# Optimization experiments

Hardware: AMD Instinct MI355X
Metric: run time of the kernel (lower is better)

Reference implementation:

```python
import jax, jax.numpy as jnp
import numpy as np

N_USERS = 50000; N_ENT = 100000; C = 64
E = 1500000; NNZ = 1000000
N_REL = 16; N_CATES = 32; NF = 4; NH = 2
R1 = N_REL - 1            # weight rows (devoted branch)
R2 = N_CATES + N_REL - 1  # weight_d rows (diverse branch)


def setup_inputs():
    key = jax.random.key(0)
    ks = list(jax.random.split(key, 32))
    f = jnp.float32
    inp = {}
    inp["user_emb"] = jax.random.normal(ks[0], (N_USERS, C), f)
    inp["entity_emb"] = jax.random.normal(ks[1], (N_ENT, C), f)
    inp["latent_emb"] = jax.random.normal(ks[2], (NF, C), f)
    inp["latent_div_emb"] = jax.random.normal(ks[3], (NF, C), f)
    inp["weight"] = jax.random.normal(ks[4], (R1, C), f) * 0.1
    inp["weight_d"] = jax.random.normal(ks[5], (R2, C), f) * 0.1
    # per-hop Aggregator params stacked over hops [NH, ...]; Linear applied as x @ W + b
    def p(k, shape, s=0.1):
        return jax.random.normal(k, shape, f) * s
    inp["cW1"] = p(ks[6], (NH, C, C)); inp["cb1"] = jnp.zeros((NH, C), f)
    inp["cW2"] = p(ks[7], (NH, C, C)); inp["cb2"] = jnp.zeros((NH, C), f)
    inp["cWua"] = p(ks[8], (NH, NF, NF)); inp["cbua"] = jnp.zeros((NH, NF), f)
    inp["cWwa"] = p(ks[9], (NH, R1, R1)); inp["cbwa"] = jnp.zeros((NH, R1), f)
    inp["eW1"] = p(ks[10], (NH, C, C)); inp["eb1"] = jnp.zeros((NH, C), f)
    inp["eW2"] = p(ks[11], (NH, C, C)); inp["eb2"] = jnp.zeros((NH, C), f)
    inp["eWua"] = p(ks[12], (NH, NF, NF)); inp["ebua"] = jnp.zeros((NH, NF), f)
    inp["eWwa"] = p(ks[13], (NH, R2, R2)); inp["ebwa"] = jnp.zeros((NH, R2), f)
    inp["interact_vals"] = jax.random.uniform(ks[14], (NNZ,), f)
    inp["edge_index"] = jax.random.randint(ks[15], (2, E), 0, N_ENT)
    inp["edge_type"] = jax.random.randint(ks[16], (E,), 1, N_REL)            # values in [1, R1]
    inp["entity_cate_set"] = jax.random.randint(ks[17], (N_ENT,), 1, N_CATES + 1)
    inp["interact_rows"] = jax.random.randint(ks[18], (NNZ,), 0, N_USERS)
    inp["interact_cols"] = jax.random.randint(ks[19], (NNZ,), 0, N_ENT)
    return inp


def _lin(x, W, b):
    return x @ W + b


def _mlp(x, W, b):  # Linear + LeakyReLU(0.2)
    return jax.nn.leaky_relu(_lin(x, W, b), 0.2)


def _normalize(x):  # F.normalize along dim=1 (eps=1e-12)
    return x / jnp.maximum(jnp.linalg.norm(x, axis=1, keepdims=True), 1e-12)


def _agg(entity_emb, user_emb, latent_emb, weight, w_idx, head, tail,
         rows, cols, vals, W1, b1, W2, b2, Wua, bua, Wwa, bwa):
    n_ent, n_usr = entity_emb.shape[0], user_emb.shape[0]
    # KG aggregate: gather -> multiply -> scatter_mean over head
    neigh = entity_emb[tail] * weight[w_idx]                                  # [E, C]
    ssum = jax.ops.segment_sum(neigh, head, num_segments=n_ent)
    cnt = jax.ops.segment_sum(jnp.ones((head.shape[0],), entity_emb.dtype), head, num_segments=n_ent)
    entity_agg = ssum / jnp.maximum(cnt, 1.0)[:, None]
    # user aggregate: sparse.mm(interact_mat, entity_emb)
    user_agg = jax.ops.segment_sum(vals[:, None] * entity_emb[cols], rows, num_segments=n_usr)
    # user -> latent interest attention
    score_ = _lin(user_emb, W1, b1) @ _lin(latent_emb, W1, b1).T              # [U, NF]
    score = jax.nn.softmax(_mlp(score_, Wua, bua), axis=1)                    # [U, NF]
    score_rp = _lin(latent_emb, W2, b2) @ _lin(weight, W2, b2).T              # [NF, R]
    latent_new = jax.nn.softmax(_mlp(score_rp, Wwa, bwa), axis=-1) @ weight   # [NF, C]
    mix = jnp.einsum("uf,fc->uc", score, latent_new)                          # (disen_weight * score).sum(1)
    user_agg = user_agg * mix + user_agg
    return entity_agg, user_agg, latent_new


def _dist_corr(t1, t2):
    ch = t1.shape[0]
    t1 = t1[:, None]; t2 = t2[:, None]
    sq1, sq2 = t1 ** 2, t2 ** 2
    a = jnp.sqrt(jnp.maximum(sq1 - 2.0 * (t1 @ t1.T) + sq1.T, 0.0) + 1e-8)
    b = jnp.sqrt(jnp.maximum(sq2 - 2.0 * (t2 @ t2.T) + sq2.T, 0.0) + 1e-8)
    A = a - a.mean(0, keepdims=True) - a.mean(1, keepdims=True) + a.mean()
    B = b - b.mean(0, keepdims=True) - b.mean(1, keepdims=True) + b.mean()
    n2 = float(ch * ch)
    dab = jnp.sqrt(jnp.maximum((A * B).sum() / n2, 0.0) + 1e-8)
    daa = jnp.sqrt(jnp.maximum((A * A).sum() / n2, 0.0) + 1e-8)
    dbb = jnp.sqrt(jnp.maximum((B * B).sum() / n2, 0.0) + 1e-8)
    return dab / jnp.sqrt(daa * dbb + 1e-8)


def _cor(lat):  # ind == "distance": sum over factor pairs
    c = jnp.asarray(0.0, lat.dtype)
    for i in range(NF):
        for j in range(i + 1, NF):
            c = c + _dist_corr(lat[i], lat[j])
    return c


def reference(user_emb, entity_emb, latent_emb, latent_div_emb, weight, weight_d,
              cW1, cb1, cW2, cb2, cWua, cbua, cWwa, cbwa,
              eW1, eb1, eW2, eb2, eWua, ebua, eWwa, ebwa,
              interact_vals, edge_index, edge_type, entity_cate_set,
              interact_rows, interact_cols):
    head, tail = edge_index[0], edge_index[1]
    idx_c = edge_type - 1               # devoted branch: relation weight index
    idx_d = entity_cate_set[tail] - 1   # diverse branch: category weight index
    # Devoted Interest Branch
    e, u, l = entity_emb, user_emb, latent_emb
    e_res, u_res, l_res = entity_emb, user_emb, latent_emb
    for i in range(NH):
        e, u, l = _agg(e, u, l, weight, idx_c, head, tail,
                       interact_rows, interact_cols, interact_vals,
                       cW1[i], cb1[i], cW2[i], cb2[i], cWua[i], cbua[i], cWwa[i], cbwa[i])
        e = _normalize(e); u = _normalize(u)
        l_res = _normalize(l)           # faithful: overwritten each hop, then += l
        e_res = e_res + e; u_res = u_res + u; l_res = l_res + l
    # Diverse Interest Branch
    e, u, l2 = entity_emb, user_emb, latent_div_emb
    e_d, u_d, l_d = entity_emb, user_emb, latent_div_emb
    for i in range(NH):
        e, u, l2 = _agg(e, u, l2, weight_d, idx_d, head, tail,
                        interact_rows, interact_cols, interact_vals,
                        eW1[i], eb1[i], eW2[i], eb2[i], eWua[i], ebua[i], eWwa[i], ebwa[i])
        e = _normalize(e); u = _normalize(u); l2 = _normalize(l2)
        e_d = e_d + e; u_d = u_d + u; l_d = l_d + l2
    cor = _cor(l_res)
    cor_d = _cor(l_d)
    return (e_res, u_res, cor, e_d, u_d, cor_d)
```

## Files before the change

### kernel.cpp

```cpp
#include <hip/hip_runtime.h>
#include <hip/hip_bf16.h>
#include <math.h>

typedef __hip_bfloat16 bf16;

#define NUSR 50000
#define NENT 100000
#define CC   64
#define EE   1500000
#define NNZI 1000000
#define NF_  4
#define R1_  15
#define R2_  47

__device__ __forceinline__ float b2f(bf16 x){ return __bfloat162float(x); }
__device__ __forceinline__ bf16  f2b(float x){ return __float2bfloat16(x); }
__device__ __forceinline__ float fin(float x){ return (x==x && fabsf(x) < 1e30f) ? x : 0.f; }

__device__ __forceinline__ unsigned bf16bits(float x){
    unsigned b = __float_as_uint(x);
    return (b + 0x7FFFu + ((b >> 16) & 1u)) >> 16;
}
__device__ __forceinline__ float pk_lo(unsigned p){ return __uint_as_float(p << 16); }
__device__ __forceinline__ float pk_hi(unsigned p){ return __uint_as_float(p & 0xFFFF0000u); }

__device__ __forceinline__ unsigned rflu(unsigned x){ return (unsigned)__builtin_amdgcn_readfirstlane((int)x); }

__device__ __forceinline__ float ldv(const float* p, long long i){ return p[i]; }
__device__ __forceinline__ float ldv(const bf16*  p, long long i){ return b2f(p[i]); }

struct LatArgs {
    const float *lin, *W1, *b1, *W2, *b2, *Wua, *bua, *Wwa, *bwa, *wt;
    float *lat, *nlat, *P2, *q2;
    int R;
};

__global__ void k_init(int* deg_e, int* deg_u, int* ctrs){
    int i = blockIdx.x*256 + threadIdx.x;
    if (i < NENT) deg_e[i] = 0;
    if (i < NUSR) deg_u[i] = 0;
    if (i < 2) ctrs[i] = 0;
}

__global__ void k_conv(const float* __restrict__ src, bf16* __restrict__ dst){
    int i = blockIdx.x*256 + threadIdx.x;
    if (i < NENT*CC) dst[i] = f2b(src[i]);
}

__global__ void k_hist(const int* __restrict__ head, const int* __restrict__ irows,
                       int* deg_e, int* deg_u,
                       int* __restrict__ rank_e, int* __restrict__ rank_u){
    int i = blockIdx.x*256 + threadIdx.x;
    if (i < EE){
        int h = head[i];
        int r = ((unsigned)h < NENT) ? atomicAdd(&deg_e[h], 1) : 0;
        rank_e[i] = r;
    } else {
        int j = i - EE;
        if (j < NNZI){
            int rr = irows[j];
            int r = ((unsigned)rr < NUSR) ? atomicAdd(&deg_u[rr], 1) : 0;
            rank_u[j] = r;
        }
    }
}

__global__ void k_base2(const int* __restrict__ deg_e, const int* __restrict__ deg_u,
                        unsigned* rsdeg_e, unsigned* rsdeg_u, int* ctrs){
    int i = blockIdx.x*256 + threadIdx.x;
    int lane = threadIdx.x & 63;
    {
        int d = (i < NENT) ? deg_e[i] : 0;
        int incl = d;
        for (int off = 1; off < 64; off <<= 1){
            int v = __shfl_up(incl, off, 64);
            if (lane >= off) incl += v;
        }
        int tot = __shfl(incl, 63, 64);
        int base = 0;
        if (lane == 63) base = atomicAdd(&ctrs[0], tot);
        base = __shfl(base, 63, 64);
        if (i < NENT){
            unsigned rs = (unsigned)(base + incl - d);
            int dc = d < 2047 ? d : 2047;
            rsdeg_e[i] = (rs & 0x1FFFFFu) | ((unsigned)dc << 21);
        }
    }
    {
        int d = (i < NUSR) ? deg_u[i] : 0;
        int incl = d;
        for (int off = 1; off < 64; off <<= 1){
            int v = __shfl_up(incl, off, 64);
            if (lane >= off) incl += v;
        }
        int tot = __shfl(incl, 63, 64);
        int base = 0;
        if (lane == 63) base = atomicAdd(&ctrs[1], tot);
        base = __shfl(base, 63, 64);
        if (i < NUSR){
            unsigned rs = (unsigned)(base + incl - d);
            int dc = d < 4095 ? d : 4095;
            rsdeg_u[i] = (rs & 0xFFFFFu) | ((unsigned)dc << 20);
        }
    }
}

__global__ void k_scatter(const int* __restrict__ head, const int* __restrict__ tail,
                          const int* __restrict__ etype, const int* __restrict__ cate,
                          const int* __restrict__ irows, const int* __restrict__ icols,
                          const float* __restrict__ ivals,
                          const int* __restrict__ rank_e, const int* __restrict__ rank_u,
                          const unsigned* __restrict__ rsdeg_e, const unsigned* __restrict__ rsdeg_u,
                          unsigned* __restrict__ epk, unsigned* __restrict__ upk){
    int i = blockIdx.x*256 + threadIdx.x;
    if (i < EE){
        int h = head[i]; if ((unsigned)h >= NENT) return;
        unsigned tu = (unsigned)tail[i]; if (tu >= NENT) tu = 0;
        int slot = (int)(rsdeg_e[h] & 0x1FFFFFu) + rank_e[i];
        unsigned ty = (unsigned)(etype[i] - 1) & 15u;
        unsigned cd = (unsigned)(cate[tu]  - 1) & 31u;
        if ((unsigned)slot < EE)
            epk[slot] = tu | (ty << 17) | (cd << 21);
    } else {
        int j = i - EE;
        if (j < NNZI){
            int r = irows[j]; if ((unsigned)r >= NUSR) return;
            unsigned c = (unsigned)icols[j]; if (c >= NENT) c = 0;
            int slot = (int)(rsdeg_u[r] & 0xFFFFFu) + rank_u[j];
            unsigned bits = __float_as_uint(ivals[j]);
            unsigned rb = bits + 0x7FFFu + ((bits >> 16) & 1u);
            unsigned vb = (rb >> 16) & 0x7FFFu;
            if ((unsigned)slot < NNZI)
                upk[slot] = c | (vb << 17);
        }
    }
}

__global__ void k_lat2(LatArgs A0, LatArgs A1){
    LatArgs a = (blockIdx.x == 0) ? A0 : A1;
    const int R = a.R;
    __shared__ float sW1[64*64], sW2[64*64];
    __shared__ float swt[R2_*64], wp[R2_*64];
    __shared__ float lf[NF_*64], lp1[NF_*64], lp2[NF_*64];
// ... 137 lines not shown
                                              const unsigned* __restrict__ rsdeg_e,
                                              const unsigned* __restrict__ epk,
                                              bf16* dst){
    __shared__ float wl[R2_*64];
    int t = threadIdx.x;
    for (int idx = t; idx < R2_*64; idx += 256)
        wl[idx] = (idx < R*64) ? wtab[idx] : 0.f;
    __syncthreads();
    int ent = blockIdx.x*4 + (t >> 6);
    int lane = t & 63;
    if (ent >= NENT) return;
    float v = ent_row(e_src, wl, epk, rsdeg_e[ent], use_d, lane);
    dst[(long long)ent*64 + lane] = f2b(v);
}

__global__ __launch_bounds__(256) void k_ent0f2(const bf16* __restrict__ ebf,
                                                const float* __restrict__ wt_c,
                                                const float* __restrict__ wt_d,
                                                const unsigned* __restrict__ rsdeg_e,
                                                const unsigned* __restrict__ epk,
                                                unsigned* __restrict__ eA2){
    __shared__ float wlc[R1_*64];
    __shared__ float wld[R2_*64];
    int t = threadIdx.x;
    for (int idx = t; idx < R1_*64; idx += 256) wlc[idx] = wt_c[idx];
    for (int idx = t; idx < R2_*64; idx += 256) wld[idx] = wt_d[idx];
    __syncthreads();
    int ent = blockIdx.x*4 + (t >> 6);
    int lane = t & 63;
    if (ent >= NENT) return;
    unsigned rd = rflu(rsdeg_e[ent]);
    int s = (int)(rd & 0x1FFFFFu);
    int deg = (int)(rd >> 21);
    int e_ = s + deg;
    float ac = 0.f, ad = 0.f;
    int k = s;
    for (; k + 4 <= e_; k += 4){
        unsigned p0 = rflu(epk[k]), p1 = rflu(epk[k+1]), p2 = rflu(epk[k+2]), p3 = rflu(epk[k+3]);
        unsigned t0 = p0 & 0x1FFFFu; t0 = t0 < NENT ? t0 : 0u;
        unsigned t1 = p1 & 0x1FFFFu; t1 = t1 < NENT ? t1 : 0u;
        unsigned t2 = p2 & 0x1FFFFu; t2 = t2 < NENT ? t2 : 0u;
        unsigned t3 = p3 & 0x1FFFFu; t3 = t3 < NENT ? t3 : 0u;
        float g0 = b2f(ebf[(long long)t0*64 + lane]);
        float g1 = b2f(ebf[(long long)t1*64 + lane]);
        float g2 = b2f(ebf[(long long)t2*64 + lane]);
        float g3 = b2f(ebf[(long long)t3*64 + lane]);
        ac += g0*wlc[((p0>>17)&15u)*64+lane] + g1*wlc[((p1>>17)&15u)*64+lane]
            + g2*wlc[((p2>>17)&15u)*64+lane] + g3*wlc[((p3>>17)&15u)*64+lane];
        ad += g0*wld[((p0>>21)&31u)*64+lane] + g1*wld[((p1>>21)&31u)*64+lane]
            + g2*wld[((p2>>21)&31u)*64+lane] + g3*wld[((p3>>21)&31u)*64+lane];
    }
    for (; k < e_; k++){
        unsigned p = rflu(epk[k]);
        unsigned ti = p & 0x1FFFFu; ti = ti < NENT ? ti : 0u;
        float g = b2f(ebf[(long long)ti*64 + lane]);
        ac += g*wlc[((p>>17)&15u)*64+lane];
        ad += g*wld[((p>>21)&31u)*64+lane];
    }
    float inv_deg = 1.f / fmaxf((float)deg, 1.f);
    float ec = fin(ac) * inv_deg, ed = fin(ad) * inv_deg;
    float sc = ec*ec, sd = ed*ed;
    for (int m = 1; m < 64; m <<= 1){
        sc += __shfl_xor(sc, m, 64);
        sd += __shfl_xor(sd, m, 64);
    }
    float vc = ec / fmaxf(sqrtf(fin(sc)), 1e-12f);
    float vd = ed / fmaxf(sqrtf(fin(sd)), 1e-12f);
    eA2[(long long)ent*64 + lane] = bf16bits(vc) | (bf16bits(vd) << 16);
}

__global__ __launch_bounds__(256) void k_ent1f(const bf16* __restrict__ e_src,
                                               const float* __restrict__ base_emb,
                                               const float* __restrict__ wtab, int R, int use_d,
                                               const unsigned* __restrict__ rsdeg_e,
                                               const unsigned* __restrict__ epk,
                                               float* dst){
    __shared__ float wl[R2_*64];
    int t = threadIdx.x;
    for (int idx = t; idx < R2_*64; idx += 256)
        wl[idx] = (idx < R*64) ? wtab[idx] : 0.f;
    __syncthreads();
    int ent = blockIdx.x*4 + (t >> 6);
    int lane = t & 63;
    if (ent >= NENT) return;
    float v = ent_row(e_src, wl, epk, rsdeg_e[ent], use_d, lane);
    long long ix = (long long)ent*64 + lane;
    dst[ix] = base_emb[ix] + b2f(e_src[ix]) + v;
}

__global__ __launch_bounds__(256) void k_ent1f2(const unsigned* __restrict__ eA2,
                                                const float* __restrict__ base_emb,
                                                const float* __restrict__ wt_c,
                                                const float* __restrict__ wt_d,
                                                const unsigned* __restrict__ rsdeg_e,
                                                const unsigned* __restrict__ epk,
                                                float* __restrict__ dst_c,
                                                float* __restrict__ dst_d){
    __shared__ float wlc[R1_*64];
    __shared__ float wld[R2_*64];
    int t = threadIdx.x;
    for (int idx = t; idx < R1_*64; idx += 256) wlc[idx] = wt_c[idx];
    for (int idx = t; idx < R2_*64; idx += 256) wld[idx] = wt_d[idx];
    __syncthreads();
    int ent = blockIdx.x*4 + (t >> 6);
    int lane = t & 63;
    if (ent >= NENT) return;
    unsigned rd = rflu(rsdeg_e[ent]);
    int s = (int)(rd & 0x1FFFFFu);
    int deg = (int)(rd >> 21);
    int e_ = s + deg;
    float ac = 0.f, ad = 0.f;
    int k = s;
    for (; k + 4 <= e_; k += 4){
        unsigned p0 = rflu(epk[k]), p1 = rflu(epk[k+1]), p2 = rflu(epk[k+2]), p3 = rflu(epk[k+3]);
        unsigned t0 = p0 & 0x1FFFFu; t0 = t0 < NENT ? t0 : 0u;
        unsigned t1 = p1 & 0x1FFFFu; t1 = t1 < NENT ? t1 : 0u;
        unsigned t2 = p2 & 0x1FFFFu; t2 = t2 < NENT ? t2 : 0u;
        unsigned t3 = p3 & 0x1FFFFu; t3 = t3 < NENT ? t3 : 0u;
        unsigned v0 = eA2[(long long)t0*64 + lane];
        unsigned v1 = eA2[(long long)t1*64 + lane];
        unsigned v2 = eA2[(long long)t2*64 + lane];
        unsigned v3 = eA2[(long long)t3*64 + lane];
        ac += pk_lo(v0)*wlc[((p0>>17)&15u)*64+lane] + pk_lo(v1)*wlc[((p1>>17)&15u)*64+lane]
            + pk_lo(v2)*wlc[((p2>>17)&15u)*64+lane] + pk_lo(v3)*wlc[((p3>>17)&15u)*64+lane];
        ad += pk_hi(v0)*wld[((p0>>21)&31u)*64+lane] + pk_hi(v1)*wld[((p1>>21)&31u)*64+lane]
            + pk_hi(v2)*wld[((p2>>21)&31u)*64+lane] + pk_hi(v3)*wld[((p3>>21)&31u)*64+lane];
    }
    for (; k < e_; k++){
        unsigned p = rflu(epk[k]);
        unsigned ti = p & 0x1FFFFu; ti = ti < NENT ? ti : 0u;
        unsigned v = eA2[(long long)ti*64 + lane];
        ac += pk_lo(v) * wlc[((p>>17)&15u)*64+lane];
        ad += pk_hi(v) * wld[((p>>21)&31u)*64+lane];
    }
    float inv_deg = 1.f / fmaxf((float)deg, 1.f);
    float vc = fin(ac) * inv_deg, vd = fin(ad) * inv_deg;
    float sc = vc*vc, sd = vd*vd;
    for (int m = 1; m < 64; m <<= 1){
        sc += __shfl_xor(sc, m, 64);
        sd += __shfl_xor(sd, m, 64);
    }
    long long ix = (long long)ent*64 + lane;
    float be = base_emb[ix];
    unsigned selfv = eA2[ix];
    dst_c[ix] = be + pk_lo(selfv) + vc / fmaxf(sqrtf(fin(sc)), 1e-12f);
    dst_d[ix] = be + pk_hi(selfv) + vd / fmaxf(sqrtf(fin(sd)), 1e-12f);
}

template<typename ESRC>
__device__ __forceinline__ float usr_gather(const ESRC* __restrict__ e_src,
                                            const unsigned* __restrict__ upk,
                                            unsigned rd, int lane){
    rd = rflu(rd);
    int s = (int)(rd & 0xFFFFFu);
    int e_ = s + (int)(rd >> 20);
    float acc = 0.f;
    int k = s;
    for (; k + 4 <= e_; k += 4){
        unsigned p0 = rflu(upk[k]), p1 = rflu(upk[k+1]), p2 = rflu(upk[k+2]), p3 = rflu(upk[k+3]);
        unsigned c0 = p0 & 0x1FFFFu; c0 = c0 < NENT ? c0 : 0u;
        unsigned c1 = p1 & 0x1FFFFu; c1 = c1 < NENT ? c1 : 0u;
// ... 50 lines not shown
                                              const float* __restrict__ lat_new,
                                              float* dst){
    __shared__ float P2l[NF_*64], latl[NF_*64], q2l[NF_];
    int t = threadIdx.x;
    P2l[t] = fin(P2[t]); latl[t] = fin(lat_new[t]);
    if (t < NF_) q2l[t] = fin(q2[t]);
    __syncthreads();
    int u = blockIdx.x*4 + (t >> 6);
    int lane = t & 63;
    if (u >= NUSR) return;
    float acc = usr_gather(e_src, upk, rsdeg_u[u], lane);
    float x = u_src[(long long)u*64 + lane];
    dst[(long long)u*64 + lane] = usr_epi(acc, x, P2l, latl, q2l, lane);
}

__global__ __launch_bounds__(256) void k_usr0f2(const float* __restrict__ u_src,
                                                const bf16* __restrict__ ebf,
                                                const unsigned* __restrict__ rsdeg_u,
                                                const unsigned* __restrict__ upk,
                                                const float* __restrict__ P2c,
                                                const float* __restrict__ q2c,
                                                const float* __restrict__ latc,
                                                const float* __restrict__ P2d,
                                                const float* __restrict__ q2d,
                                                const float* __restrict__ latd,
                                                float* __restrict__ dst_c,
                                                float* __restrict__ dst_d){
    __shared__ float P2lc[NF_*64], latlc[NF_*64], P2ld[NF_*64], latld[NF_*64];
    __shared__ float q2lc[NF_], q2ld[NF_];
    int t = threadIdx.x;
    P2lc[t] = fin(P2c[t]); latlc[t] = fin(latc[t]);
    P2ld[t] = fin(P2d[t]); latld[t] = fin(latd[t]);
    if (t < NF_){ q2lc[t] = fin(q2c[t]); q2ld[t] = fin(q2d[t]); }
    __syncthreads();
    int u = blockIdx.x*4 + (t >> 6);
    int lane = t & 63;
    if (u >= NUSR) return;
    float acc = usr_gather(ebf, upk, rsdeg_u[u], lane);
    long long ix = (long long)u*64 + lane;
    float x = u_src[ix];
    dst_c[ix] = usr_epi(acc, x, P2lc, latlc, q2lc, lane);
    dst_d[ix] = usr_epi(acc, x, P2ld, latld, q2ld, lane);
}

__global__ __launch_bounds__(256) void k_usr1f(float* u_io,
                                               const bf16* __restrict__ e_src,
                                               const float* __restrict__ base_emb,
                                               const unsigned* __restrict__ rsdeg_u,
                                               const unsigned* __restrict__ upk,
                                               const float* __restrict__ P2,
                                               const float* __restrict__ q2,
                                               const float* __restrict__ lat_new){
    __shared__ float P2l[NF_*64], latl[NF_*64], q2l[NF_];
    int t = threadIdx.x;
    P2l[t] = fin(P2[t]); latl[t] = fin(lat_new[t]);
    if (t < NF_) q2l[t] = fin(q2[t]);
    __syncthreads();
    int u = blockIdx.x*4 + (t >> 6);
    int lane = t & 63;
    if (u >= NUSR) return;
    float acc = usr_gather(e_src, upk, rsdeg_u[u], lane);
    long long ix = (long long)u*64 + lane;
    float x = u_io[ix];
    float v = usr_epi(acc, x, P2l, latl, q2l, lane);
    u_io[ix] = base_emb[ix] + x + v;
}

__global__ __launch_bounds__(256) void k_usr1f2(float* __restrict__ uc_io,
                                                float* __restrict__ ud_io,
                                                const unsigned* __restrict__ eA2,
                                                const float* __restrict__ base_emb,
                                                const unsigned* __restrict__ rsdeg_u,
                                                const unsigned* __restrict__ upk,
                                                const float* __restrict__ P2c,
                                                const float* __restrict__ q2c,
                                                const float* __restrict__ latc,
                                                const float* __restrict__ P2d,
                                                const float* __restrict__ q2d,
                                                const float* __restrict__ latd){
    __shared__ float P2lc[NF_*64], latlc[NF_*64], P2ld[NF_*64], latld[NF_*64];
    __shared__ float q2lc[NF_], q2ld[NF_];
    int t = threadIdx.x;
    P2lc[t] = fin(P2c[t]); latlc[t] = fin(latc[t]);
    P2ld[t] = fin(P2d[t]); latld[t] = fin(latd[t]);
    if (t < NF_){ q2lc[t] = fin(q2c[t]); q2ld[t] = fin(q2d[t]); }
    __syncthreads();
    int u = blockIdx.x*4 + (t >> 6);
    int lane = t & 63;
    if (u >= NUSR) return;
    unsigned rd = rflu(rsdeg_u[u]);
    int s = (int)(rd & 0xFFFFFu);
    int e_ = s + (int)(rd >> 20);
    float accc = 0.f, accd = 0.f;
    int k = s;
    for (; k + 4 <= e_; k += 4){
        unsigned p0 = rflu(upk[k]), p1 = rflu(upk[k+1]), p2 = rflu(upk[k+2]), p3 = rflu(upk[k+3]);
        unsigned c0 = p0 & 0x1FFFFu; c0 = c0 < NENT ? c0 : 0u;
        unsigned c1 = p1 & 0x1FFFFu; c1 = c1 < NENT ? c1 : 0u;
        unsigned c2 = p2 & 0x1FFFFu; c2 = c2 < NENT ? c2 : 0u;
        unsigned c3 = p3 & 0x1FFFFu; c3 = c3 < NENT ? c3 : 0u;
        float v0 = __uint_as_float(((p0 >> 17) & 0x7FFFu) << 16);
        float v1 = __uint_as_float(((p1 >> 17) & 0x7FFFu) << 16);
        float v2 = __uint_as_float(((p2 >> 17) & 0x7FFFu) << 16);
        float v3 = __uint_as_float(((p3 >> 17) & 0x7FFFu) << 16);
        unsigned g0 = eA2[(long long)c0*64 + lane];
        unsigned g1 = eA2[(long long)c1*64 + lane];
        unsigned g2 = eA2[(long long)c2*64 + lane];
        unsigned g3 = eA2[(long long)c3*64 + lane];
        accc += v0*pk_lo(g0) + v1*pk_lo(g1) + v2*pk_lo(g2) + v3*pk_lo(g3);
        accd += v0*pk_hi(g0) + v1*pk_hi(g1) + v2*pk_hi(g2) + v3*pk_hi(g3);
    }
    for (; k < e_; k++){
        unsigned p = rflu(upk[k]);
        unsigned c = p & 0x1FFFFu; c = c < NENT ? c : 0u;
        float v = __uint_as_float(((p >> 17) & 0x7FFFu) << 16);
        unsigned g = eA2[(long long)c*64 + lane];
        accc += v * pk_lo(g);
        accd += v * pk_hi(g);
    }
    long long ix = (long long)u*64 + lane;
    float xc = uc_io[ix], xd = ud_io[ix];
    float be = base_emb[ix];
    float vc = usr_epi(fin(accc), xc, P2lc, latlc, q2lc, lane);
    float vd = usr_epi(fin(accd), xd, P2ld, latld, q2ld, lane);
    uc_io[ix] = be + xc + vc;
    ud_io[ix] = be + xd + vd;
}

__global__ void k_cor(const float* __restrict__ latn1_c,
                      const float* __restrict__ ldiv,
                      const float* __restrict__ nld0, const float* __restrict__ nld1,
                      float* out){
    __shared__ float rows[NF_*64];
    __shared__ float nr[NF_];
    __shared__ float t1s[64], t2s[64], m1s[64], m2s[64];
    __shared__ float pr[256], pr2[256], pr3[256];
    __shared__ float gms[2];
    __shared__ float corsh;
    int t = threadIdx.x, b = blockIdx.x;

    if (b == 0){
// ... 116 lines not shown
    size_t ebuf  = (size_t)NENT*CC*2;
    size_t ebuf2 = (size_t)NENT*CC*4;
    bool tierA = (ws_size >= common + ((ebuf + 255) & ~(size_t)255) + ((ebuf2 + 255) & ~(size_t)255));

    bf16 *ebf = nullptr; unsigned* eA2 = nullptr; bf16* eA = nullptr;
    char* scratch_base;
    if (tierA){
        ebf = (bf16*)carve(ebuf);
        eA2 = (unsigned*)carve(ebuf2);
        scratch_base = (char*)eA2;
    } else {
        eA  = (bf16*)carve(ebuf);
        scratch_base = (char*)eA;
    }

    int* deg_e = (int*)scratch_base;
    int* deg_u = (int*)(scratch_base + (512<<10));
    int* ctrs  = (int*)(scratch_base + (1024<<10));
    char* rbase = scratch_base + (1280<<10);
    int* rank_e = (int*)rbase;
    int* rank_u = (int*)(rbase + (((size_t)EE*4 + 255) & ~(size_t)255));

    float* oe_c = out;
    float* ou_c = out + 6400000LL;
    float* oe_d = out + 9600001LL;
    float* ou_d = out + 16000001LL;

    k_init<<<(NENT+255)/256, 256, 0, stream>>>(deg_e, deg_u, ctrs);
    if (tierA) k_conv<<<(NENT*CC+255)/256, 256, 0, stream>>>(entity_emb, ebf);
    int gh = (EE + NNZI + 255)/256;
    k_hist<<<gh, 256, 0, stream>>>(head, irows, deg_e, deg_u, rank_e, rank_u);
    k_base2<<<(NENT+255)/256, 256, 0, stream>>>(deg_e, deg_u, rsdeg_e, rsdeg_u, ctrs);
    k_scatter<<<gh, 256, 0, stream>>>(head, tail, etype, cate, irows, icols, ivals,
                                      rank_e, rank_u, rsdeg_e, rsdeg_u, epk, upk);

    LatArgs a_c0 = {latent_emb, cW1, cb1, cW2, cb2, cWua, cbua, cWwa, cbwa, weight,
                    latn[0][0], nlat[0][0], P2b[0][0], q2b[0][0], R1_};
    LatArgs a_d0 = {latent_div, eW1, eb1, eW2, eb2, eWua, ebua, eWwa, ebwa, weight_d,
                    latn[1][0], nlat[1][0], P2b[1][0], q2b[1][0], R2_};
    k_lat2<<<2, 256, 0, stream>>>(a_c0, a_d0);
    LatArgs a_c1 = {latn[0][0], cW1+4096, cb1+64, cW2+4096, cb2+64, cWua+16, cbua+4,
                    cWwa+R1_*R1_, cbwa+R1_, weight,
                    latn[0][1], nlat[0][1], P2b[0][1], q2b[0][1], R1_};
    LatArgs a_d1 = {nlat[1][0], eW1+4096, eb1+64, eW2+4096, eb2+64, eWua+16, ebua+4,
                    eWwa+R2_*R2_, ebwa+R2_, weight_d,
                    latn[1][1], nlat[1][1], P2b[1][1], q2b[1][1], R2_};
    k_lat2<<<2, 256, 0, stream>>>(a_c1, a_d1);

    int ge = (NENT+3)/4, gu = (NUSR+3)/4;
    if (tierA){
        k_ent0f2<<<ge, 256, 0, stream>>>(ebf, weight, weight_d, rsdeg_e, epk, eA2);
        k_usr0f2<<<gu, 256, 0, stream>>>(user_emb, ebf, rsdeg_u, upk,
            P2b[0][0], q2b[0][0], latn[0][0],
            P2b[1][0], q2b[1][0], latn[1][0], ou_c, ou_d);
        k_ent1f2<<<ge, 256, 0, stream>>>(eA2, entity_emb, weight, weight_d,
                                         rsdeg_e, epk, oe_c, oe_d);
        k_usr1f2<<<gu, 256, 0, stream>>>(ou_c, ou_d, eA2, user_emb, rsdeg_u, upk,
            P2b[0][1], q2b[0][1], latn[0][1],
            P2b[1][1], q2b[1][1], latn[1][1]);
    } else {
        const float* wts[2] = {weight, weight_d};
        const int    Rs[2]  = {R1_, R2_};
        float* oes[2] = {oe_c, oe_d};
        float* ous[2] = {ou_c, ou_d};
        for (int br = 0; br < 2; br++){
            k_ent0<<<ge, 256, 0, stream>>>(entity_emb, wts[br], Rs[br], br, rsdeg_e, epk, eA);
            k_usr0<<<gu, 256, 0, stream>>>(user_emb, entity_emb, rsdeg_u, upk,
                P2b[br][0], q2b[br][0], latn[br][0], ous[br]);
            k_ent1f<<<ge, 256, 0, stream>>>(eA, entity_emb, wts[br], Rs[br], br, rsdeg_e, epk, oes[br]);
            k_usr1f<<<gu, 256, 0, stream>>>(ous[br], eA, user_emb, rsdeg_u, upk,
                P2b[br][1], q2b[br][1], latn[br][1]);
        }
// ... 5 lines not shown
```

Measured before the change: 851.0 us.

## Shard degree histogram atomics and merge entity/user hop kernels into single launches

Degree counting now uses eight sharded counter arrays chosen by block index, which spreads atomic contention, and ranks are stored as 16-bit values carrying the shard id. The base kernel turns the shard counts into per-shard offsets that the scatter kernel adds back. The separate entity and user kernels for each hop are merged into one launch that branches on block index, so the entity and user work can run concurrently and fewer launches are issued. Costs are extra zero-init and memory traffic for the sharded counters, and a rank limit of 8191 per shard per row.

Measured after the change: 833.5 us. 1.02x faster.

```diff
diff --git a/kernel.cpp b/kernel.cpp
--- a/kernel.cpp
+++ b/kernel.cpp
@@ -3,6 +3,7 @@
 #include <math.h>
 
 typedef __hip_bfloat16 bf16;
+typedef unsigned short u16;
 
 #define NUSR 50000
 #define NENT 100000
@@ -12,6 +13,7 @@
 #define NF_  4
 #define R1_  15
 #define R2_  47
+#define NSH  8
 
 __device__ __forceinline__ float b2f(bf16 x){ return __bfloat162float(x); }
 __device__ __forceinline__ bf16  f2b(float x){ return __float2bfloat16(x); }
@@ -35,10 +37,10 @@
     int R;
 };
 
-__global__ void k_init(int* deg_e, int* deg_u, int* ctrs){
+__global__ void k_init(int* deg8_e, int* deg8_u, int* ctrs){
     int i = blockIdx.x*256 + threadIdx.x;
-    if (i < NENT) deg_e[i] = 0;
-    if (i < NUSR) deg_u[i] = 0;
+    if (i < NSH*NENT) deg8_e[i] = 0;
+    if (i < NSH*NUSR) deg8_u[i] = 0;
     if (i < 2) ctrs[i] = 0;
 }
 
@@ -48,29 +50,40 @@
 }
 
 __global__ void k_hist(const int* __restrict__ head, const int* __restrict__ irows,
-                       int* deg_e, int* deg_u,
-                       int* __restrict__ rank_e, int* __restrict__ rank_u){
+                       int* deg8_e, int* deg8_u,
+                       u16* __restrict__ rank_e, u16* __restrict__ rank_u){
     int i = blockIdx.x*256 + threadIdx.x;
+    int shard = blockIdx.x & (NSH-1);
     if (i < EE){
         int h = head[i];
-        int r = ((unsigned)h < NENT) ? atomicAdd(&deg_e[h], 1) : 0;
-        rank_e[i] = r;
+        int r = ((unsigned)h < NENT) ? atomicAdd(&deg8_e[shard*NENT + h], 1) : 0;
+        rank_e[i] = (u16)((r & 8191) | (shard << 13));
     } else {
         int j = i - EE;
         if (j < NNZI){
             int rr = irows[j];
-            int r = ((unsigned)rr < NUSR) ? atomicAdd(&deg_u[rr], 1) : 0;
-            rank_u[j] = r;
-        }
-    }
-}
-
-__global__ void k_base2(const int* __restrict__ deg_e, const int* __restrict__ deg_u,
+            int r = ((unsigned)rr < NUSR) ? atomicAdd(&deg8_u[shard*NUSR + rr], 1) : 0;
+            rank_u[j] = (u16)((r & 8191) | (shard << 13));
+        }
+    }
+}
+
+__global__ void k_base2(int* deg8_e, int* deg8_u,
                         unsigned* rsdeg_e, unsigned* rsdeg_u, int* ctrs){
     int i = blockIdx.x*256 + threadIdx.x;
     int lane = threadIdx.x & 63;
     {
-        int d = (i < NENT) ? deg_e[i] : 0;
+        int d = 0;
+        if (i < NENT){
+            int tot = 0;
+            #pragma unroll
+            for (int c = 0; c < NSH; c++){
+                int v = deg8_e[c*NENT + i];
+                deg8_e[c*NENT + i] = tot;
+                tot += v;
+            }
+            d = tot;
+        }
         int incl = d;
         for (int off = 1; off < 64; off <<= 1){
             int v = __shfl_up(incl, off, 64);
@@ -87,7 +100,17 @@
         }
     }
     {
-        int d = (i < NUSR) ? deg_u[i] : 0;
+        int d = 0;
+        if (i < NUSR){
+            int tot = 0;
+            #pragma unroll
+            for (int c = 0; c < NSH; c++){
+                int v = deg8_u[c*NUSR + i];
+                deg8_u[c*NUSR + i] = tot;
+                tot += v;
+            }
+            d = tot;
+        }
         int incl = d;
         for (int off = 1; off < 64; off <<= 1){
             int v = __shfl_up(incl, off, 64);
@@ -109,14 +132,17 @@
                           const int* __restrict__ etype, const int* __restrict__ cate,
                           const int* __restrict__ irows, const int* __restrict__ icols,
                           const float* __restrict__ ivals,
-                          const int* __restrict__ rank_e, const int* __restrict__ rank_u,
+                          const u16* __restrict__ rank_e, const u16* __restrict__ rank_u,
+                          const int* __restrict__ xoff_e, const int* __restrict__ xoff_u,
                           const unsigned* __restrict__ rsdeg_e, const unsigned* __restrict__ rsdeg_u,
                           unsigned* __restrict__ epk, unsigned* __restrict__ upk){
     int i = blockIdx.x*256 + threadIdx.x;
     if (i < EE){
         int h = head[i]; if ((unsigned)h >= NENT) return;
         unsigned tu = (unsigned)tail[i]; if (tu >= NENT) tu = 0;
-        int slot = (int)(rsdeg_e[h] & 0x1FFFFFu) + rank_e[i];
+        unsigned rk = rank_e[i];
+        int shard = rk >> 13, r = rk & 8191;
+        int slot = (int)(rsdeg_e[h] & 0x1FFFFFu) + xoff_e[shard*NENT + h] + r;
         unsigned ty = (unsigned)(etype[i] - 1) & 15u;
         unsigned cd = (unsigned)(cate[tu]  - 1) & 31u;
         if ((unsigned)slot < EE)
@@ -124,9 +150,11 @@
     } else {
         int j = i - EE;
         if (j < NNZI){
-            int r = irows[j]; if ((unsigned)r >= NUSR) return;
+            int rr = irows[j]; if ((unsigned)rr >= NUSR) return;
             unsigned c = (unsigned)icols[j]; if (c >= NENT) c = 0;
-            int slot = (int)(rsdeg_u[r] & 0xFFFFFu) + rank_u[j];
+            unsigned rk = rank_u[j];
+            int shard = rk >> 13, r = rk & 8191;
+            int slot = (int)(rsdeg_u[rr] & 0xFFFFFu) + xoff_u[shard*NUSR + rr] + r;
             unsigned bits = __float_as_uint(ivals[j]);
             unsigned rb = bits + 0x7FFFu + ((bits >> 16) & 1u);
             unsigned vb = (rb >> 16) & 0x7FFFu;
@@ -294,61 +322,6 @@
     dst[(long long)ent*64 + lane] = f2b(v);
 }
 
-__global__ __launch_bounds__(256) void k_ent0f2(const bf16* __restrict__ ebf,
-                                                const float* __restrict__ wt_c,
-                                                const float* __restrict__ wt_d,
-                                                const unsigned* __restrict__ rsdeg_e,
-                                                const unsigned* __restrict__ epk,
-                                                unsigned* __restrict__ eA2){
-    __shared__ float wlc[R1_*64];
-    __shared__ float wld[R2_*64];
-    int t = threadIdx.x;
-    for (int idx = t; idx < R1_*64; idx += 256) wlc[idx] = wt_c[idx];
-    for (int idx = t; idx < R2_*64; idx += 256) wld[idx] = wt_d[idx];
-    __syncthreads();
-    int ent = blockIdx.x*4 + (t >> 6);
-    int lane = t & 63;
-    if (ent >= NENT) return;
-    unsigned rd = rflu(rsdeg_e[ent]);
-    int s = (int)(rd & 0x1FFFFFu);
-    int deg = (int)(rd >> 21);
-    int e_ = s + deg;
-    float ac = 0.f, ad = 0.f;
-    int k = s;
-    for (; k + 4 <= e_; k += 4){
-        unsigned p0 = rflu(epk[k]), p1 = rflu(epk[k+1]), p2 = rflu(epk[k+2]), p3 = rflu(epk[k+3]);
-        unsigned t0 = p0 & 0x1FFFFu; t0 = t0 < NENT ? t0 : 0u;
-        unsigned t1 = p1 & 0x1FFFFu; t1 = t1 < NENT ? t1 : 0u;
-        unsigned t2 = p2 & 0x1FFFFu; t2 = t2 < NENT ? t2 : 0u;
-        unsigned t3 = p3 & 0x1FFFFu; t3 = t3 < NENT ? t3 : 0u;
-        float g0 = b2f(ebf[(long long)t0*64 + lane]);
-        float g1 = b2f(ebf[(long long)t1*64 + lane]);
-        float g2 = b2f(ebf[(long long)t2*64 + lane]);
-        float g3 = b2f(ebf[(long long)t3*64 + lane]);
-        ac += g0*wlc[((p0>>17)&15u)*64+lane] + g1*wlc[((p1>>17)&15u)*64+lane]
-            + g2*wlc[((p2>>17)&15u)*64+lane] + g3*wlc[((p3>>17)&15u)*64+lane];
-        ad += g0*wld[((p0>>21)&31u)*64+lane] + g1*wld[((p1>>21)&31u)*64+lane]
-            + g2*wld[((p2>>21)&31u)*64+lane] + g3*wld[((p3>>21)&31u)*64+lane];
-    }
-    for (; k < e_; k++){
-        unsigned p = rflu(epk[k]);
-        unsigned ti = p & 0x1FFFFu; ti = ti < NENT ? ti : 0u;
-        float g = b2f(ebf[(long long)ti*64 + lane]);
-        ac += g*wlc[((p>>17)&15u)*64+lane];
-        ad += g*wld[((p>>21)&31u)*64+lane];
-    }
-    float inv_deg = 1.f / fmaxf((float)deg, 1.f);
-    float ec = fin(ac) * inv_deg, ed = fin(ad) * inv_deg;
-    float sc = ec*ec, sd = ed*ed;
-    for (int m = 1; m < 64; m <<= 1){
-        sc += __shfl_xor(sc, m, 64);
-        sd += __shfl_xor(sd, m, 64);
-    }
-    float vc = ec / fmaxf(sqrtf(fin(sc)), 1e-12f);
-    float vd = ed / fmaxf(sqrtf(fin(sd)), 1e-12f);
-    eA2[(long long)ent*64 + lane] = bf16bits(vc) | (bf16bits(vd) << 16);
-}
-
 __global__ __launch_bounds__(256) void k_ent1f(const bf16* __restrict__ e_src,
                                                const float* __restrict__ base_emb,
                                                const float* __restrict__ wtab, int R, int use_d,
@@ -366,65 +339,6 @@
     float v = ent_row(e_src, wl, epk, rsdeg_e[ent], use_d, lane);
     long long ix = (long long)ent*64 + lane;
     dst[ix] = base_emb[ix] + b2f(e_src[ix]) + v;
-}
-
-__global__ __launch_bounds__(256) void k_ent1f2(const unsigned* __restrict__ eA2,
-                                                const float* __restrict__ base_emb,
-                                                const float* __restrict__ wt_c,
-                                                const float* __restrict__ wt_d,
-                                                const unsigned* __restrict__ rsdeg_e,
-                                                const unsigned* __restrict__ epk,
-                                                float* __restrict__ dst_c,
-                                                float* __restrict__ dst_d){
-    __shared__ float wlc[R1_*64];
-    __shared__ float wld[R2_*64];
-    int t = threadIdx.x;
-    for (int idx = t; idx < R1_*64; idx += 256) wlc[idx] = wt_c[idx];
-    for (int idx = t; idx < R2_*64; idx += 256) wld[idx] = wt_d[idx];
-    __syncthreads();
-    int ent = blockIdx.x*4 + (t >> 6);
-    int lane = t & 63;
-    if (ent >= NENT) return;
-    unsigned rd = rflu(rsdeg_e[ent]);
-    int s = (int)(rd & 0x1FFFFFu);
-    int deg = (int)(rd >> 21);
-    int e_ = s + deg;
-    float ac = 0.f, ad = 0.f;
-    int k = s;
-    for (; k + 4 <= e_; k += 4){
-        unsigned p0 = rflu(epk[k]), p1 = rflu(epk[k+1]), p2 = rflu(epk[k+2]), p3 = rflu(epk[k+3]);
-        unsigned t0 = p0 & 0x1FFFFu; t0 = t0 < NENT ? t0 : 0u;
-        unsigned t1 = p1 & 0x1FFFFu; t1 = t1 < NENT ? t1 : 0u;
-        unsigned t2 = p2 & 0x1FFFFu; t2 = t2 < NENT ? t2 : 0u;
-        unsigned t3 = p3 & 0x1FFFFu; t3 = t3 < NENT ? t3 : 0u;
-        unsigned v0 = eA2[(long long)t0*64 + lane];
-        unsigned v1 = eA2[(long long)t1*64 + lane];
-        unsigned v2 = eA2[(long long)t2*64 + lane];
-        unsigned v3 = eA2[(long long)t3*64 + lane];
-        ac += pk_lo(v0)*wlc[((p0>>17)&15u)*64+lane] + pk_lo(v1)*wlc[((p1>>17)&15u)*64+lane]
-            + pk_lo(v2)*wlc[((p2>>17)&15u)*64+lane] + pk_lo(v3)*wlc[((p3>>17)&15u)*64+lane];
-        ad += pk_hi(v0)*wld[((p0>>21)&31u)*64+lane] + pk_hi(v1)*wld[((p1>>21)&31u)*64+lane]
-            + pk_hi(v2)*wld[((p2>>21)&31u)*64+lane] + pk_hi(v3)*wld[((p3>>21)&31u)*64+lane];
-    }
-    for (; k < e_; k++){
-        unsigned p = rflu(epk[k]);
-        unsigned ti = p & 0x1FFFFu; ti = ti < NENT ? ti : 0u;
-        unsigned v = eA2[(long long)ti*64 + lane];
-        ac += pk_lo(v) * wlc[((p>>17)&15u)*64+lane];
-        ad += pk_hi(v) * wld[((p>>21)&31u)*64+lane];
-    }
-    float inv_deg = 1.f / fmaxf((float)deg, 1.f);
-    float vc = fin(ac) * inv_deg, vd = fin(ad) * inv_deg;
-    float sc = vc*vc, sd = vd*vd;
-    for (int m = 1; m < 64; m <<= 1){
-        sc += __shfl_xor(sc, m, 64);
-        sd += __shfl_xor(sd, m, 64);
-    }
-    long long ix = (long long)ent*64 + lane;
-    float be = base_emb[ix];
-    unsigned selfv = eA2[ix];
-    dst_c[ix] = be + pk_lo(selfv) + vc / fmaxf(sqrtf(fin(sc)), 1e-12f);
-    dst_d[ix] = be + pk_hi(selfv) + vd / fmaxf(sqrtf(fin(sd)), 1e-12f);
 }
 
 template<typename ESRC>
@@ -505,35 +419,6 @@
     dst[(long long)u*64 + lane] = usr_epi(acc, x, P2l, latl, q2l, lane);
 }
 
-__global__ __launch_bounds__(256) void k_usr0f2(const float* __restrict__ u_src,
-                                                const bf16* __restrict__ ebf,
-                                                const unsigned* __restrict__ rsdeg_u,
-                                                const unsigned* __restrict__ upk,
-                                                const float* __restrict__ P2c,
-                                                const float* __restrict__ q2c,
-                                                const float* __restrict__ latc,
-                                                const float* __restrict__ P2d,
-                                                const float* __restrict__ q2d,
-                                                const float* __restrict__ latd,
-                                                float* __restrict__ dst_c,
-                                                float* __restrict__ dst_d){
-    __shared__ float P2lc[NF_*64], latlc[NF_*64], P2ld[NF_*64], latld[NF_*64];
-    __shared__ float q2lc[NF_], q2ld[NF_];
-    int t = threadIdx.x;
-    P2lc[t] = fin(P2c[t]); latlc[t] = fin(latc[t]);
-    P2ld[t] = fin(P2d[t]); latld[t] = fin(latd[t]);
-    if (t < NF_){ q2lc[t] = fin(q2c[t]); q2ld[t] = fin(q2d[t]); }
-    __syncthreads();
-    int u = blockIdx.x*4 + (t >> 6);
-    int lane = t & 63;
-    if (u >= NUSR) return;
-    float acc = usr_gather(ebf, upk, rsdeg_u[u], lane);
-    long long ix = (long long)u*64 + lane;
-    float x = u_src[ix];
-    dst_c[ix] = usr_epi(acc, x, P2lc, latlc, q2lc, lane);
-    dst_d[ix] = usr_epi(acc, x, P2ld, latld, q2ld, lane);
-}
-
 __global__ __launch_bounds__(256) void k_usr1f(float* u_io,
                                                const bf16* __restrict__ e_src,
                                                const float* __restrict__ base_emb,
@@ -557,65 +442,216 @@
     u_io[ix] = base_emb[ix] + x + v;
 }
 
-__global__ __launch_bounds__(256) void k_usr1f2(float* __restrict__ uc_io,
-                                                float* __restrict__ ud_io,
-                                                const unsigned* __restrict__ eA2,
-                                                const float* __restrict__ base_emb,
-                                                const unsigned* __restrict__ rsdeg_u,
-                                                const unsigned* __restrict__ upk,
-                                                const float* __restrict__ P2c,
-                                                const float* __restrict__ q2c,
-                                                const float* __restrict__ latc,
-                                                const float* __restrict__ P2d,
-                                                const float* __restrict__ q2d,
-                                                const float* __restrict__ latd){
-    __shared__ float P2lc[NF_*64], latlc[NF_*64], P2ld[NF_*64], latld[NF_*64];
-    __shared__ float q2lc[NF_], q2ld[NF_];
+#define GE_ ((NENT+3)/4)
+#define GU_ ((NUSR+3)/4)
+__global__ __launch_bounds__(256) void k_it0(const bf16* __restrict__ ebf,
+                                             const float* __restrict__ wt_c,
+                                             const float* __restrict__ wt_d,
+                                             const unsigned* __restrict__ rsdeg_e,
+                                             const unsigned* __restrict__ epk,
+                                             unsigned* __restrict__ eA2,
+                                             const float* __restrict__ u_src,
+                                             const unsigned* __restrict__ rsdeg_u,
+                                             const unsigned* __restrict__ upk,
+                                             const float* __restrict__ P2c,
+                                             const float* __restrict__ q2c,
+                                             const float* __restrict__ latc,
+                                             const float* __restrict__ P2d,
+                                             const float* __restrict__ q2d,
+                                             const float* __restrict__ latd,
+                                             float* __restrict__ dst_c,
+                                             float* __restrict__ dst_d){
+    __shared__ float sm[(R1_+R2_)*64];
     int t = threadIdx.x;
-    P2lc[t] = fin(P2c[t]); latlc[t] = fin(latc[t]);
-    P2ld[t] = fin(P2d[t]); latld[t] = fin(latd[t]);
-    if (t < NF_){ q2lc[t] = fin(q2c[t]); q2ld[t] = fin(q2d[t]); }
-    __syncthreads();
-    int u = blockIdx.x*4 + (t >> 6);
     int lane = t & 63;
-    if (u >= NUSR) return;
-    unsigned rd = rflu(rsdeg_u[u]);
-    int s = (int)(rd & 0xFFFFFu);
-    int e_ = s + (int)(rd >> 20);
-    float accc = 0.f, accd = 0.f;
-    int k = s;
-    for (; k + 4 <= e_; k += 4){
-        unsigned p0 = rflu(upk[k]), p1 = rflu(upk[k+1]), p2 = rflu(upk[k+2]), p3 = rflu(upk[k+3]);
-        unsigned c0 = p0 & 0x1FFFFu; c0 = c0 < NENT ? c0 : 0u;
-        unsigned c1 = p1 & 0x1FFFFu; c1 = c1 < NENT ? c1 : 0u;
-        unsigned c2 = p2 & 0x1FFFFu; c2 = c2 < NENT ? c2 : 0u;
-        unsigned c3 = p3 & 0x1FFFFu; c3 = c3 < NENT ? c3 : 0u;
-        float v0 = __uint_as_float(((p0 >> 17) & 0x7FFFu) << 16);
-        float v1 = __uint_as_float(((p1 >> 17) & 0x7FFFu) << 16);
-        float v2 = __uint_as_float(((p2 >> 17) & 0x7FFFu) << 16);
-        float v3 = __uint_as_float(((p3 >> 17) & 0x7FFFu) << 16);
-        unsigned g0 = eA2[(long long)c0*64 + lane];
-        unsigned g1 = eA2[(long long)c1*64 + lane];
-        unsigned g2 = eA2[(long long)c2*64 + lane];
-        unsigned g3 = eA2[(long long)c3*64 + lane];
-        accc += v0*pk_lo(g0) + v1*pk_lo(g1) + v2*pk_lo(g2) + v3*pk_lo(g3);
-        accd += v0*pk_hi(g0) + v1*pk_hi(g1) + v2*pk_hi(g2) + v3*pk_hi(g3);
-    }
-    for (; k < e_; k++){
-        unsigned p = rflu(upk[k]);
-        unsigned c = p & 0x1FFFFu; c = c < NENT ? c : 0u;
-        float v = __uint_as_float(((p >> 17) & 0x7FFFu) << 16);
-        unsigned g = eA2[(long long)c*64 + lane];
-        accc += v * pk_lo(g);
-        accd += v * pk_hi(g);
-    }
-    long long ix = (long long)u*64 + lane;
-    float xc = uc_io[ix], xd = ud_io[ix];
-    float be = base_emb[ix];
-    float vc = usr_epi(fin(accc), xc, P2lc, latlc, q2lc, lane);
-    float vd = usr_epi(fin(accd), xd, P2ld, latld, q2ld, lane);
-    uc_io[ix] = be + xc + vc;
-    ud_io[ix] = be + xd + vd;
+    if (blockIdx.x < GE_){
+        float* wlc = sm;
+        float* wld = sm + R1_*64;
+        for (int idx = t; idx < R1_*64; idx += 256) wlc[idx] = wt_c[idx];
+        for (int idx = t; idx < R2_*64; idx += 256) wld[idx] = wt_d[idx];
+        __syncthreads();
+        int ent = blockIdx.x*4 + (t >> 6);
+        if (ent >= NENT) return;
+        unsigned rd = rflu(rsdeg_e[ent]);
+        int s = (int)(rd & 0x1FFFFFu);
+        int deg = (int)(rd >> 21);
+        int e_ = s + deg;
+        float ac = 0.f, ad = 0.f;
+        int k = s;
+        for (; k + 4 <= e_; k += 4){
+            unsigned p0 = rflu(epk[k]), p1 = rflu(epk[k+1]), p2 = rflu(epk[k+2]), p3 = rflu(epk[k+3]);
+            unsigned t0 = p0 & 0x1FFFFu; t0 = t0 < NENT ? t0 : 0u;
+            unsigned t1 = p1 & 0x1FFFFu; t1 = t1 < NENT ? t1 : 0u;
+            unsigned t2 = p2 & 0x1FFFFu; t2 = t2 < NENT ? t2 : 0u;
+            unsigned t3 = p3 & 0x1FFFFu; t3 = t3 < NENT ? t3 : 0u;
+            float g0 = b2f(ebf[(long long)t0*64 + lane]);
+            float g1 = b2f(ebf[(long long)t1*64 + lane]);
+            float g2 = b2f(ebf[(long long)t2*64 + lane]);
+            float g3 = b2f(ebf[(long long)t3*64 + lane]);
+            ac += g0*wlc[((p0>>17)&15u)*64+lane] + g1*wlc[((p1>>17)&15u)*64+lane]
+                + g2*wlc[((p2>>17)&15u)*64+lane] + g3*wlc[((p3>>17)&15u)*64+lane];
+            ad += g0*wld[((p0>>21)&31u)*64+lane] + g1*wld[((p1>>21)&31u)*64+lane]
+                + g2*wld[((p2>>21)&31u)*64+lane] + g3*wld[((p3>>21)&31u)*64+lane];
+        }
+        for (; k < e_; k++){
+            unsigned p = rflu(epk[k]);
+            unsigned ti = p & 0x1FFFFu; ti = ti < NENT ? ti : 0u;
+            float g = b2f(ebf[(long long)ti*64 + lane]);
+            ac += g*wlc[((p>>17)&15u)*64+lane];
+            ad += g*wld[((p>>21)&31u)*64+lane];
+        }
+        float inv_deg = 1.f / fmaxf((float)deg, 1.f);
+        float ec = fin(ac) * inv_deg, ed = fin(ad) * inv_deg;
+        float sc = ec*ec, sd = ed*ed;
+        for (int m = 1; m < 64; m <<= 1){
+            sc += __shfl_xor(sc, m, 64);
+            sd += __shfl_xor(sd, m, 64);
+        }
+        float vc = ec / fmaxf(sqrtf(fin(sc)), 1e-12f);
+        float vd = ed / fmaxf(sqrtf(fin(sd)), 1e-12f);
+        eA2[(long long)ent*64 + lane] = bf16bits(vc) | (bf16bits(vd) << 16);
+    } else {
+        float* P2lc = sm;
+        float* latlc = sm + 256;
+        float* P2ld = sm + 512;
+        float* latld = sm + 768;
+        float* q2lc = sm + 1024;
+        float* q2ld = sm + 1032;
+        P2lc[t] = fin(P2c[t]); latlc[t] = fin(latc[t]);
+        P2ld[t] = fin(P2d[t]); latld[t] = fin(latd[t]);
+        if (t < NF_){ q2lc[t] = fin(q2c[t]); q2ld[t] = fin(q2d[t]); }
+        __syncthreads();
+        int u = (blockIdx.x - GE_)*4 + (t >> 6);
+        if (u >= NUSR) return;
+        float acc = usr_gather(ebf, upk, rsdeg_u[u], lane);
+        long long ix = (long long)u*64 + lane;
+        float x = u_src[ix];
+        dst_c[ix] = usr_epi(acc, x, P2lc, latlc, q2lc, lane);
+        dst_d[ix] = usr_epi(acc, x, P2ld, latld, q2ld, lane);
+    }
+}
+
+__global__ __launch_bounds__(256) void k_it1(const unsigned* __restrict__ eA2,
+                                             const float* __restrict__ ent_base,
+                                             const float* __restrict__ wt_c,
+                                             const float* __restrict__ wt_d,
+                                             const unsigned* __restrict__ rsdeg_e,
+                                             const unsigned* __restrict__ epk,
+                                             float* __restrict__ oe_c,
+                                             float* __restrict__ oe_d,
+                                             float* __restrict__ uc_io,
+                                             float* __restrict__ ud_io,
+                                             const float* __restrict__ usr_base,
+                                             const unsigned* __restrict__ rsdeg_u,
+                                             const unsigned* __restrict__ upk,
+                                             const float* __restrict__ P2c,
+                                             const float* __restrict__ q2c,
+                                             const float* __restrict__ latc,
+                                             const float* __restrict__ P2d,
+                                             const float* __restrict__ q2d,
+                                             const float* __restrict__ latd){
+    __shared__ float sm[(R1_+R2_)*64];
+    int t = threadIdx.x;
+    int lane = t & 63;
+    if (blockIdx.x < GE_){
+        float* wlc = sm;
+        float* wld = sm + R1_*64;
+        for (int idx = t; idx < R1_*64; idx += 256) wlc[idx] = wt_c[idx];
+        for (int idx = t; idx < R2_*64; idx += 256) wld[idx] = wt_d[idx];
+        __syncthreads();
+        int ent = blockIdx.x*4 + (t >> 6);
+        if (ent >= NENT) return;
+        unsigned rd = rflu(rsdeg_e[ent]);
+        int s = (int)(rd & 0x1FFFFFu);
+        int deg = (int)(rd >> 21);
+        int e_ = s + deg;
+        float ac = 0.f, ad = 0.f;
+        int k = s;
+        for (; k + 4 <= e_; k += 4){
+            unsigned p0 = rflu(epk[k]), p1 = rflu(epk[k+1]), p2 = rflu(epk[k+2]), p3 = rflu(epk[k+3]);
+            unsigned t0 = p0 & 0x1FFFFu; t0 = t0 < NENT ? t0 : 0u;
+            unsigned t1 = p1 & 0x1FFFFu; t1 = t1 < NENT ? t1 : 0u;
+            unsigned t2 = p2 & 0x1FFFFu; t2 = t2 < NENT ? t2 : 0u;
+            unsigned t3 = p3 & 0x1FFFFu; t3 = t3 < NENT ? t3 : 0u;
+            unsigned v0 = eA2[(long long)t0*64 + lane];
+            unsigned v1 = eA2[(long long)t1*64 + lane];
+            unsigned v2 = eA2[(long long)t2*64 + lane];
+            unsigned v3 = eA2[(long long)t3*64 + lane];
+            ac += pk_lo(v0)*wlc[((p0>>17)&15u)*64+lane] + pk_lo(v1)*wlc[((p1>>17)&15u)*64+lane]
+                + pk_lo(v2)*wlc[((p2>>17)&15u)*64+lane] + pk_lo(v3)*wlc[((p3>>17)&15u)*64+lane];
+            ad += pk_hi(v0)*wld[((p0>>21)&31u)*64+lane] + pk_hi(v1)*wld[((p1>>21)&31u)*64+lane]
+                + pk_hi(v2)*wld[((p2>>21)&31u)*64+lane] + pk_hi(v3)*wld[((p3>>21)&31u)*64+lane];
+        }
+        for (; k < e_; k++){
+            unsigned p = rflu(epk[k]);
+            unsigned ti = p & 0x1FFFFu; ti = ti < NENT ? ti : 0u;
+            unsigned v = eA2[(long long)ti*64 + lane];
+            ac += pk_lo(v) * wlc[((p>>17)&15u)*64+lane];
+            ad += pk_hi(v) * wld[((p>>21)&31u)*64+lane];
+        }
+        float inv_deg = 1.f / fmaxf((float)deg, 1.f);
+        float vc = fin(ac) * inv_deg, vd = fin(ad) * inv_deg;
+        float sc = vc*vc, sd = vd*vd;
+        for (int m = 1; m < 64; m <<= 1){
+            sc += __shfl_xor(sc, m, 64);
+            sd += __shfl_xor(sd, m, 64);
+        }
+        long long ix = (long long)ent*64 + lane;
+        float be = ent_base[ix];
+        unsigned selfv = eA2[ix];
+        oe_c[ix] = be + pk_lo(selfv) + vc / fmaxf(sqrtf(fin(sc)), 1e-12f);
+        oe_d[ix] = be + pk_hi(selfv) + vd / fmaxf(sqrtf(fin(sd)), 1e-12f);
+    } else {
+        float* P2lc = sm;
+        float* latlc = sm + 256;
+        float* P2ld = sm + 512;
+        float* latld = sm + 768;
+        float* q2lc = sm + 1024;
+        float* q2ld = sm + 1032;
+        P2lc[t] = fin(P2c[t]); latlc[t] = fin(latc[t]);
+        P2ld[t] = fin(P2d[t]); latld[t] = fin(latd[t]);
+        if (t < NF_){ q2lc[t] = fin(q2c[t]); q2ld[t] = fin(q2d[t]); }
+        __syncthreads();
+        int u = (blockIdx.x - GE_)*4 + (t >> 6);
+        if (u >= NUSR) return;
+        unsigned rd = rflu(rsdeg_u[u]);
+        int s = (int)(rd & 0xFFFFFu);
+        int e_ = s + (int)(rd >> 20);
+        float accc = 0.f, accd = 0.f;
+        int k = s;
+        for (; k + 4 <= e_; k += 4){
+            unsigned p0 = rflu(upk[k]), p1 = rflu(upk[k+1]), p2 = rflu(upk[k+2]), p3 = rflu(upk[k+3]);
+            unsigned c0 = p0 & 0x1FFFFu; c0 = c0 < NENT ? c0 : 0u;
+            unsigned c1 = p1 & 0x1FFFFu; c1 = c1 < NENT ? c1 : 0u;
+            unsigned c2 = p2 & 0x1FFFFu; c2 = c2 < NENT ? c2 : 0u;
+            unsigned c3 = p3 & 0x1FFFFu; c3 = c3 < NENT ? c3 : 0u;
+            float v0 = __uint_as_float(((p0 >> 17) & 0x7FFFu) << 16);
+            float v1 = __uint_as_float(((p1 >> 17) & 0x7FFFu) << 16);
+            float v2 = __uint_as_float(((p2 >> 17) & 0x7FFFu) << 16);
+            float v3 = __uint_as_float(((p3 >> 17) & 0x7FFFu) << 16);
+            unsigned g0 = eA2[(long long)c0*64 + lane];
+            unsigned g1 = eA2[(long long)c1*64 + lane];
+            unsigned g2 = eA2[(long long)c2*64 + lane];
+            unsigned g3 = eA2[(long long)c3*64 + lane];
+            accc += v0*pk_lo(g0) + v1*pk_lo(g1) + v2*pk_lo(g2) + v3*pk_lo(g3);
+            accd += v0*pk_hi(g0) + v1*pk_hi(g1) + v2*pk_hi(g2) + v3*pk_hi(g3);
+        }
+        for (; k < e_; k++){
+            unsigned p = rflu(upk[k]);
+            unsigned c = p & 0x1FFFFu; c = c < NENT ? c : 0u;
+            float v = __uint_as_float(((p >> 17) & 0x7FFFu) << 16);
+            unsigned g = eA2[(long long)c*64 + lane];
+            accc += v * pk_lo(g);
+            accd += v * pk_hi(g);
+        }
+        long long ix = (long long)u*64 + lane;
+        float xc = uc_io[ix], xd = ud_io[ix];
+        float be = usr_base[ix];
+        float vc = usr_epi(fin(accc), xc, P2lc, latlc, q2lc, lane);
+        float vd = usr_epi(fin(accd), xd, P2ld, latld, q2ld, lane);
+        uc_io[ix] = be + xc + vc;
+        ud_io[ix] = be + xd + vd;
+    }
 }
 
 __global__ void k_cor(const float* __restrict__ latn1_c,
@@ -762,25 +798,26 @@
         scratch_base = (char*)eA;
     }
 
-    int* deg_e = (int*)scratch_base;
-    int* deg_u = (int*)(scratch_base + (512<<10));
-    int* ctrs  = (int*)(scratch_base + (1024<<10));
-    char* rbase = scratch_base + (1280<<10);
-    int* rank_e = (int*)rbase;
-    int* rank_u = (int*)(rbase + (((size_t)EE*4 + 255) & ~(size_t)255));
+    int* deg8_e = (int*)scratch_base;
+    int* deg8_u = (int*)(scratch_base + 3276800);
+    int* ctrs   = (int*)(scratch_base + 4915200);
+    u16* rank_e = (u16*)(scratch_base + 5242880);
+    u16* rank_u = (u16*)(scratch_base + 8388608);
 
     float* oe_c = out;
     float* ou_c = out + 6400000LL;
     float* oe_d = out + 9600001LL;
     float* ou_d = out + 16000001LL;
 
-    k_init<<<(NENT+255)/256, 256, 0, stream>>>(deg_e, deg_u, ctrs);
+    int gi = (NSH*NENT + 255)/256;
+    k_init<<<gi, 256, 0, stream>>>(deg8_e, deg8_u, ctrs);
     if (tierA) k_conv<<<(NENT*CC+255)/256, 256, 0, stream>>>(entity_emb, ebf);
     int gh = (EE + NNZI + 255)/256;
-    k_hist<<<gh, 256, 0, stream>>>(head, irows, deg_e, deg_u, rank_e, rank_u);
-    k_base2<<<(NENT+255)/256, 256, 0, stream>>>(deg_e, deg_u, rsdeg_e, rsdeg_u, ctrs);
+    k_hist<<<gh, 256, 0, stream>>>(head, irows, deg8_e, deg8_u, rank_e, rank_u);
+    k_base2<<<(NENT+255)/256, 256, 0, stream>>>(deg8_e, deg8_u, rsdeg_e, rsdeg_u, ctrs);
     k_scatter<<<gh, 256, 0, stream>>>(head, tail, etype, cate, irows, icols, ivals,
-                                      rank_e, rank_u, rsdeg_e, rsdeg_u, epk, upk);
+                                      rank_e, rank_u, deg8_e, deg8_u,
+                                      rsdeg_e, rsdeg_u, epk, upk);
 
     LatArgs a_c0 = {latent_emb, cW1, cb1, cW2, cb2, cWua, cbua, cWwa, cbwa, weight,
                     latn[0][0], nlat[0][0], P2b[0][0], q2b[0][0], R1_};
@@ -795,15 +832,15 @@
                     latn[1][1], nlat[1][1], P2b[1][1], q2b[1][1], R2_};
     k_lat2<<<2, 256, 0, stream>>>(a_c1, a_d1);
 
-    int ge = (NENT+3)/4, gu = (NUSR+3)/4;
+    int ge = GE_, gu = GU_;
     if (tierA){
-        k_ent0f2<<<ge, 256, 0, stream>>>(ebf, weight, weight_d, rsdeg_e, epk, eA2);
-        k_usr0f2<<<gu, 256, 0, stream>>>(user_emb, ebf, rsdeg_u, upk,
+        k_it0<<<ge + gu, 256, 0, stream>>>(ebf, weight, weight_d, rsdeg_e, epk, eA2,
+            user_emb, rsdeg_u, upk,
             P2b[0][0], q2b[0][0], latn[0][0],
             P2b[1][0], q2b[1][0], latn[1][0], ou_c, ou_d);
-        k_ent1f2<<<ge, 256, 0, stream>>>(eA2, entity_emb, weight, weight_d,
-                                         rsdeg_e, epk, oe_c, oe_d);
-        k_usr1f2<<<gu, 256, 0, stream>>>(ou_c, ou_d, eA2, user_emb, rsdeg_u, upk,
+        k_it1<<<ge + gu, 256, 0, stream>>>(eA2, entity_emb, weight, weight_d,
+            rsdeg_e, epk, oe_c, oe_d,
+            ou_c, ou_d, user_emb, rsdeg_u, upk,
             P2b[0][1], q2b[0][1], latn[0][1],
             P2b[1][1], q2b[1][1], latn[1][1]);
     } else {
```
